# Performance work log

Measured on AMD Instinct MI355X. Metric: run time of the kernel, lower is better.

## Reference

```python
import jax, jax.numpy as jnp
import numpy as np

N_ATOMS = 100000
N_BONDS = 250000
MAX_NB = 6
HIDDEN = 256
DEPTH = 3
NUM_MOLS = 2000
ATOM_FDIM = 133
BOND_FDIM = 147


def setup_inputs() -> dict:
    key = jax.random.key(0)
    ks = jax.random.split(key, 12)
    return {
        "f_atoms": jax.random.normal(ks[0], (N_ATOMS, ATOM_FDIM), jnp.float32),
        "f_bonds": jax.random.normal(ks[1], (N_BONDS, BOND_FDIM), jnp.float32),
        "w_atoms": jax.random.uniform(ks[2], (N_ATOMS,), jnp.float32),
        "w_bonds": jax.random.uniform(ks[3], (N_BONDS,), jnp.float32),
        "W_i": jax.random.normal(ks[4], (BOND_FDIM, HIDDEN), jnp.float32) * 0.05,
        "W_h": jax.random.normal(ks[5], (HIDDEN, HIDDEN), jnp.float32) * 0.05,
        "W_o": jax.random.normal(ks[6], (ATOM_FDIM + HIDDEN, HIDDEN), jnp.float32) * 0.05,
        "b_o": jnp.zeros((HIDDEN,), jnp.float32),
        "degree_of_polym": jax.random.uniform(ks[7], (NUM_MOLS,), jnp.float32),
        "a2b": jax.random.randint(ks[8], (N_ATOMS, MAX_NB), 0, N_BONDS, jnp.int32),
        "b2a": jax.random.randint(ks[9], (N_BONDS,), 0, N_ATOMS, jnp.int32),
        "b2revb": jax.random.randint(ks[10], (N_BONDS,), 0, N_BONDS, jnp.int32),
        "mol_ids": jnp.sort(jax.random.randint(ks[11], (N_ATOMS,), 0, NUM_MOLS, jnp.int32)),
    }


def reference(f_atoms, f_bonds, w_atoms, w_bonds, W_i, W_h, W_o, b_o,
              degree_of_polym, a2b, b2a, b2revb, mol_ids):
    # input-layer: bond features -> hidden messages
    inp = f_bonds @ W_i                      # [n_bonds, H]
    message = jax.nn.relu(inp)

    for _ in range(DEPTH - 1):
        # gather incoming bond messages per atom and weight them
        nei_msg = message[a2b]               # [n_atoms, max_nb, H]
        nei_w = w_bonds[a2b]                 # [n_atoms, max_nb]
        a_message = (nei_msg * nei_w[..., None]).sum(axis=1)  # [n_atoms, H]
        # directed message: total at source atom minus reverse bond
        message = a_message[b2a] - message[b2revb]             # [n_bonds, H]
        message = jax.nn.relu(inp + message @ W_h)             # dropout p=0 (eval)

    # final atom-level readout
    nei_msg = message[a2b] * w_bonds[a2b][..., None]
    a_message = nei_msg.sum(axis=1)                            # [n_atoms, H]
    a_input = jnp.concatenate([f_atoms, a_message], axis=1)    # [n_atoms, atom_fdim+H]
    atom_hiddens = jax.nn.relu(a_input @ W_o + b_o)            # [n_atoms, H]

    # per-molecule weighted mean aggregation (a_scope loop -> segment_sum)
    weighted = atom_hiddens * w_atoms[:, None]
    mol_sum = jax.ops.segment_sum(weighted, mol_ids, num_segments=NUM_MOLS)
    w_sum = jax.ops.segment_sum(w_atoms, mol_ids, num_segments=NUM_MOLS)
    safe_w = jnp.where(w_sum > 0, w_sum, 1.0)
    mol_vecs = jnp.where((w_sum > 0)[:, None], mol_sum / safe_w[:, None], 0.0)
    mol_vecs = degree_of_polym[:, None] * mol_vecs             # [num_mols, H]
    return mol_vecs
```

## Files before the change

kernel.cpp:

```cpp
#include <hip/hip_runtime.h>
#include <hip/hip_bf16.h>

typedef unsigned short u16;
typedef __bf16 bf16x8v __attribute__((ext_vector_type(8)));
typedef float f32x4v __attribute__((ext_vector_type(4)));
typedef float f32x4u __attribute__((ext_vector_type(4))) __attribute__((aligned(4)));

__device__ __forceinline__ float bf2f(u16 u) {
    union { float f; unsigned int i; } c; c.i = ((unsigned int)u) << 16; return c.f;
}
__device__ __forceinline__ u16 f2bf(float f) {
    union { float f; unsigned int i; } c; c.f = f;
    unsigned int i = c.i;
    unsigned int lsb = (i >> 16) & 1u;
    i += 0x7fffu + lsb;
    return (u16)(i >> 16);
}
__device__ __forceinline__ float lo16(unsigned u) { return bf2f((u16)(u & 0xffff)); }
__device__ __forceinline__ float hi16(unsigned u) { return bf2f((u16)(u >> 16)); }
__device__ __forceinline__ unsigned pack2(float lo, float hi) {
    return (unsigned)f2bf(lo) | ((unsigned)f2bf(hi) << 16);
}

__device__ __forceinline__ unsigned neg2(unsigned u) { return u ^ 0x80008000u; }
__device__ __forceinline__ unsigned relu_neg2(unsigned u) {
    unsigned s = u & 0x80008000u;
    unsigned m = (s - (s >> 15)) | s;
    return (u ^ 0x80008000u) & ~m;
}

__device__ __forceinline__ bf16x8v load_cvt8(const float* __restrict__ rowp, int k, int kmax) {
    union { unsigned u[4]; bf16x8v v; } r;
#pragma unroll
    for (int g = 0; g < 2; ++g) {
        int kk = k + g * 4;
        float f0, f1, f2, f3;
        if (kk + 3 < kmax) {
            f32x4u q = *(const f32x4u*)(rowp + kk);
            f0 = q.x; f1 = q.y; f2 = q.z; f3 = q.w;
        } else {
            f0 = (kk + 0 < kmax) ? rowp[kk + 0] : 0.f;
            f1 = (kk + 1 < kmax) ? rowp[kk + 1] : 0.f;
            f2 = (kk + 2 < kmax) ? rowp[kk + 2] : 0.f;
            f3 = (kk + 3 < kmax) ? rowp[kk + 3] : 0.f;
        }
        r.u[g * 2]     = pack2(f0, f1);
        r.u[g * 2 + 1] = pack2(f2, f3);
    }
    return r.v;
}

__global__ __launch_bounds__(256)
void pack_all(const float* __restrict__ W_i, const float* __restrict__ W_h,
              const float* __restrict__ W_o,
              u16* __restrict__ wti, u16* __restrict__ wth, u16* __restrict__ wto) {
    int idx = blockIdx.x * 256 + threadIdx.x;
    if (idx < 256 * 160) {
        int n = idx / 160, k = idx % 160;
        wti[idx] = f2bf(k < 147 ? W_i[k * 256 + n] : 0.f);
        return;
    }
    idx -= 256 * 160;
    if (idx < 256 * 256) {
        int n = idx / 256, k = idx % 256;
        wth[idx] = f2bf(W_h[k * 256 + n]);
        return;
    }
    idx -= 256 * 256;
    if (idx < 256 * 448) {
        int n = idx / 448, k = idx % 448;
        float v;
        if (k < 256)       v = W_o[(133 + k) * 256 + n];
        else if (k < 389)  v = W_o[(k - 256) * 256 + n];
        else               v = 0.f;
        wto[idx] = f2bf(v);
    }
}

template <bool RELU>
__global__ __launch_bounds__(256)
void gather16(const u16* __restrict__ msg, const int* __restrict__ a2b,
              const float* __restrict__ w_bonds, u16* __restrict__ out, int nAtoms) {
    int t = threadIdx.x;
    int g = t >> 5;
    int co = (t & 31) * 8;
    int atom0 = blockIdx.x * 16 + g;
    int atom1 = atom0 + 8;
    if (atom1 >= nAtoms) { if (atom0 >= nAtoms) return; atom1 = atom0; }

    int bidx[12];
#pragma unroll
    for (int j = 0; j < 6; ++j) {
        bidx[j]     = a2b[atom0 * 6 + j];
        bidx[6 + j] = a2b[atom1 * 6 + j];
    }
    float w[12];
#pragma unroll
    for (int j = 0; j < 12; ++j) w[j] = w_bonds[bidx[j]];
    uint4 v[12];
#pragma unroll
    for (int j = 0; j < 12; ++j)
        v[j] = *(const uint4*)(msg + (size_t)bidx[j] * 256 + co);

    float a0[8] = {0,0,0,0,0,0,0,0}, a1[8] = {0,0,0,0,0,0,0,0};
#pragma unroll
    for (int j = 0; j < 6; ++j) {
        unsigned p[4] = {v[j].x, v[j].y, v[j].z, v[j].w};
        unsigned q[4] = {v[6+j].x, v[6+j].y, v[6+j].z, v[6+j].w};
#pragma unroll
        for (int c = 0; c < 4; ++c) {
            float m0 = lo16(p[c]), m1 = hi16(p[c]);
            float n0 = lo16(q[c]), n1 = hi16(q[c]);
            if (RELU) {
                m0 = fmaxf(m0, 0.f); m1 = fmaxf(m1, 0.f);
                n0 = fmaxf(n0, 0.f); n1 = fmaxf(n1, 0.f);
            }
            a0[c * 2]     += w[j] * m0;
            a0[c * 2 + 1] += w[j] * m1;
            a1[c * 2]     += w[6+j] * n0;
            a1[c * 2 + 1] += w[6+j] * n1;
        }
    }
    uint4 o0, o1;
    o0.x = pack2(a0[0], a0[1]); o0.y = pack2(a0[2], a0[3]);
    o0.z = pack2(a0[4], a0[5]); o0.w = pack2(a0[6], a0[7]);
    o1.x = pack2(a1[0], a1[1]); o1.y = pack2(a1[2], a1[3]);
    o1.z = pack2(a1[4], a1[5]); o1.w = pack2(a1[6], a1[7]);
    *(uint4*)(out + (size_t)atom0 * 256 + co) = o0;
    if (atom1 != atom0)
        *(uint4*)(out + (size_t)atom1 * 256 + co) = o1;
}

__global__ __launch_bounds__(512, 2)
void gemm_in(const float* __restrict__ A, const u16* __restrict__ Bt, int M,
             u16* __restrict__ out0) {
    constexpr int KPAD = 160, KMAX = 147, ASTR = 147;
    constexpr int LSTR = KPAD + 8;
    __shared__ u16 Bs[256 * LSTR];
    const int tid = threadIdx.x;
    const int wave = tid >> 6;
    const int lane = tid & 63;
    const int mrow = lane & 15;
    const int quad = lane >> 4;

    constexpr int KC = KPAD / 8;
    for (int i = tid; i < 256 * KC; i += 512) {
        int r = i / KC, kc = i % KC;
        *(uint4*)&Bs[r * LSTR + kc * 8] = *(const uint4*)&Bt[(size_t)r * KPAD + kc * 8];
    }
    __syncthreads();

    for (long chunk = blockIdx.x; chunk * 256 < (long)M; chunk += gridDim.x) {
        const long mbase = chunk * 256 + wave * 32;
        const float* rowp[2];
#pragma unroll
        for (int t = 0; t < 2; ++t) {
            long r = mbase + t * 16 + mrow;
            if (r >= M) r = M - 1;
            rowp[t] = A + r * ASTR;
        }

        f32x4v acc[2][16];
#pragma unroll
        for (int t = 0; t < 2; ++t)
#pragma unroll
            for (int j = 0; j < 16; ++j) acc[t][j] = (f32x4v){0.f, 0.f, 0.f, 0.f};

#pragma unroll 2
        for (int k0 = 0; k0 < KPAD; k0 += 32) {
            bf16x8v a_frag[2];
#pragma unroll
            for (int t = 0; t < 2; ++t)
                a_frag[t] = load_cvt8(rowp[t], k0 + quad * 8, KMAX);
#pragma unroll
            for (int jg = 0; jg < 4; ++jg) {
                bf16x8v b_frag[4];
#pragma unroll
                for (int j4 = 0; j4 < 4; ++j4)
                    b_frag[j4] = *(const bf16x8v*)&Bs[((jg * 4 + j4) * 16 + mrow) * LSTR + k0 + quad * 8];
#pragma unroll
                for (int t = 0; t < 2; ++t)
#pragma unroll
                    for (int j4 = 0; j4 < 4; ++j4)
                        acc[t][jg * 4 + j4] = __builtin_amdgcn_mfma_f32_16x16x32_bf16(
                            a_frag[t], b_frag[j4], acc[t][jg * 4 + j4], 0, 0, 0);
            }
        }

#pragma unroll
        for (int t = 0; t < 2; ++t)
#pragma unroll
            for (int r = 0; r < 4; ++r) {
                long grow = mbase + t * 16 + quad * 4 + r;
                if (grow < M)
#pragma unroll
                    for (int j = 0; j < 16; ++j)
                        out0[(size_t)grow * 256 + j * 16 + mrow] = f2bf(acc[t][j][r]);
            }
    }
}

template <bool RELUV>
__global__ __launch_bounds__(1024, 8)
void gemm_mp(const u16* __restrict__ amsg, const u16* __restrict__ msgsrc,
             const int* __restrict__ b2a, const int* __restrict__ b2revb,
             const u16* __restrict__ Bt, int M,
             const u16* __restrict__ inp, u16* __restrict__ out0) {
    constexpr int KPAD = 256;
    constexpr int LSTR = KPAD + 8;
    constexpr int NROWS = 128;
    __shared__ u16 Bs[NROWS * LSTR];
    const int tid = threadIdx.x;
    const int wave = tid >> 6;
    const int lane = tid & 63;
    const int mrow = lane & 15;
    const int quad = lane >> 4;

    const int nch = (M + 255) >> 8;
    const int cpx = (nch + 7) >> 3;
    const int bid = blockIdx.x;
    const int xcd = bid & 7;
    const int seq = bid >> 3;
    const long chunk = (long)xcd * cpx + (seq >> 1);
    if (chunk >= nch) return;
    const int nbase = (seq & 1) * NROWS;

    for (int i = tid; i < NROWS * 32; i += 1024) {
        int r = i >> 5, kc = i & 31;
        *(uint4*)&Bs[r * LSTR + kc * 8] = *(const uint4*)&Bt[(size_t)(nbase + r) * KPAD + kc * 8];
    }
    __syncthreads();

    const long mbase = chunk * 256 + wave * 16;
    long b = mbase + mrow;
    if (b >= M) b = M - 1;
    const size_t soff = (size_t)b2a[b] * 256 + quad * 8;
    const size_t roff = (size_t)b2revb[b] * 256 + quad * 8;

    f32x4v acc[8];
#pragma unroll
    for (int j = 0; j < 8; ++j) acc[j] = (f32x4v){0.f, 0.f, 0.f, 0.f};

#pragma unroll 2
    for (int k0 = 0; k0 < KPAD; k0 += 32) {
        uint4 va = *(const uint4*)&amsg[soff + k0];
        uint4 vr = *(const uint4*)&msgsrc[roff + k0];
        union { uint4 q; bf16x8v v; } ua, ur;
        ua.q = va;
        if (RELUV) {
            ur.q.x = relu_neg2(vr.x); ur.q.y = relu_neg2(vr.y);
            ur.q.z = relu_neg2(vr.z); ur.q.w = relu_neg2(vr.w);
        } else {
            ur.q.x = neg2(vr.x); ur.q.y = neg2(vr.y);
            ur.q.z = neg2(vr.z); ur.q.w = neg2(vr.w);
        }
#pragma unroll
        for (int j = 0; j < 8; ++j) {
            bf16x8v b_frag = *(const bf16x8v*)&Bs[(j * 16 + mrow) * LSTR + k0 + quad * 8];
            acc[j] = __builtin_amdgcn_mfma_f32_16x16x32_bf16(ua.v, b_frag, acc[j], 0, 0, 0);
            acc[j] = __builtin_amdgcn_mfma_f32_16x16x32_bf16(ur.v, b_frag, acc[j], 0, 0, 0);
        }
    }

#pragma unroll
    for (int r = 0; r < 4; ++r) {
        long grow = mbase + quad * 4 + r;
        if (grow < M)
#pragma unroll
            for (int j = 0; j < 8; ++j) {
                size_t idx = (size_t)grow * 256 + nbase + j * 16 + mrow;
                float s = bf2f(inp[idx]) + acc[j][r];
                out0[idx] = f2bf(s > 0.f ? s : 0.f);
            }
    }
}

__global__ __launch_bounds__(512, 2)
void gemm_ro(const u16* __restrict__ A1, const float* __restrict__ A2,
             const u16* __restrict__ Bt, int M,
             const float* __restrict__ bias, float* __restrict__ outf) {
    constexpr int KPAD = 448, KSPLIT = 256, K2 = 192, KMAX2 = 133;
    constexpr int LSTR = KPAD + 8;
    constexpr int NROWS = 128;
    __shared__ u16 Bs[NROWS * LSTR];
    const int tid = threadIdx.x;
    const int wave = tid >> 6;
    const int lane = tid & 63;
    const int mrow = lane & 15;
    const int quad = lane >> 4;

    const int nch = (M + 255) >> 8;
    const int cpx = (nch + 7) >> 3;
    const int bid = blockIdx.x;
    const int xcd = bid & 7;
    const int seq = bid >> 3;
    const long chunk = (long)xcd * cpx + (seq >> 1);
    if (chunk >= nch) return;
    const int nbase = (seq & 1) * NROWS;

    constexpr int KC = KPAD / 8;
    for (int i = tid; i < NROWS * KC; i += 512) {
        int r = i / KC, kc = i % KC;
        *(uint4*)&Bs[r * LSTR + kc * 8] =
            *(const uint4*)&Bt[(size_t)(nbase + r) * KPAD + kc * 8];
    }
    __syncthreads();

    const long mbase = chunk * 256 + wave * 32;
    long row[2];
#pragma unroll
    for (int t = 0; t < 2; ++t) {
        long r = mbase + t * 16 + mrow;
        if (r >= M) r = M - 1;
        row[t] = r;
    }

    f32x4v acc[2][8];
#pragma unroll
    for (int t = 0; t < 2; ++t)
#pragma unroll
        for (int j = 0; j < 8; ++j) acc[t][j] = (f32x4v){0.f, 0.f, 0.f, 0.f};

#pragma unroll 2
    for (int k0 = 0; k0 < KSPLIT; k0 += 32) {
        bf16x8v a_frag[2], b_frag[8];
#pragma unroll
        for (int t = 0; t < 2; ++t)
            a_frag[t] = *(const bf16x8v*)&A1[row[t] * KSPLIT + k0 + quad * 8];
#pragma unroll
        for (int j = 0; j < 8; ++j)
            b_frag[j] = *(const bf16x8v*)&Bs[(j * 16 + mrow) * LSTR + k0 + quad * 8];
#pragma unroll
        for (int t = 0; t < 2; ++t)
#pragma unroll
            for (int j = 0; j < 8; ++j)
                acc[t][j] = __builtin_amdgcn_mfma_f32_16x16x32_bf16(
                    a_frag[t], b_frag[j], acc[t][j], 0, 0, 0);
    }
#pragma unroll 2
    for (int k0 = 0; k0 < K2; k0 += 32) {
        bf16x8v a_frag[2], b_frag[8];
#pragma unroll
        for (int t = 0; t < 2; ++t)
            a_frag[t] = load_cvt8(A2 + row[t] * KMAX2, k0 + quad * 8, KMAX2);
#pragma unroll
        for (int j = 0; j < 8; ++j)
            b_frag[j] = *(const bf16x8v*)&Bs[(j * 16 + mrow) * LSTR + KSPLIT + k0 + quad * 8];
#pragma unroll
        for (int t = 0; t < 2; ++t)
#pragma unroll
            for (int j = 0; j < 8; ++j)
                acc[t][j] = __builtin_amdgcn_mfma_f32_16x16x32_bf16(
                    a_frag[t], b_frag[j], acc[t][j], 0, 0, 0);
    }

#pragma unroll
    for (int t = 0; t < 2; ++t)
#pragma unroll
        for (int r = 0; r < 4; ++r) {
            long grow = mbase + t * 16 + quad * 4 + r;
            if (grow < M)
#pragma unroll
                for (int j = 0; j < 8; ++j) {
                    int gcol = nbase + j * 16 + mrow;
                    float s = acc[t][j][r] + bias[gcol];
                    outf[(size_t)grow * 256 + gcol] = s > 0.f ? s : 0.f;
                }
        }
}

__global__ __launch_bounds__(256)
void aggregate_kernel(const float* __restrict__ hid, const float* __restrict__ w_atoms,
                      const int* __restrict__ mol_ids, const float* __restrict__ deg,
                      float* __restrict__ out, int nAtoms) {
    int m = blockIdx.x;
    int t = threadIdx.x;
    int lo = 0, hi = nAtoms;
    while (lo < hi) { int mid = (lo + hi) >> 1; if (mol_ids[mid] < m) lo = mid + 1; else hi = mid; }
    int start = lo;
    lo = start; hi = nAtoms;
    while (lo < hi) { int mid = (lo + hi) >> 1; if (mol_ids[mid] < m + 1) lo = mid + 1; else hi = mid; }
    int end = lo;
    float acc = 0.f, wsum = 0.f;
    for (int a = start; a < end; ++a) {
        float w = w_atoms[a];
        wsum += w;
        acc += w * hid[(size_t)a * 256 + t];
    }
    float res = (wsum > 0.f) ? deg[m] * acc / wsum : 0.f;
    out[m * 256 + t] = res;
}

extern "C" void kernel_launch(void* const* d_in, const int* in_sizes, int n_in,
                              void* d_out, int out_size, void* d_ws, size_t ws_size,
                              hipStream_t stream) {
    const float* f_atoms = (const float*)d_in[0];
    const float* f_bonds = (const float*)d_in[1];
    const float* w_atoms = (const float*)d_in[2];
    const float* w_bonds = (const float*)d_in[3];
    const float* W_i     = (const float*)d_in[4];
    const float* W_h     = (const float*)d_in[5];
    const float* W_o     = (const float*)d_in[6];
    const float* b_o     = (const float*)d_in[7];
    const float* deg     = (const float*)d_in[8];
    const int*   a2b     = (const int*)d_in[9];
    const int*   b2a     = (const int*)d_in[10];
    const int*   b2revb  = (const int*)d_in[11];
    const int*   mol_ids = (const int*)d_in[12];
    float* out = (float*)d_out;

    const int nB = 250000, nA = 100000, nM = 2000;

    char* ws = (char*)d_ws;
    u16* inp    = (u16*)(ws);
    u16* msgA   = (u16*)(ws + 128000000L);
    float* hid  = (float*)(ws + 256000000L);
    u16* amsg   = (u16*)(ws + 384000000L);
    u16* wt_i   = (u16*)(ws + 435200000L);
    u16* wt_h   = (u16*)(ws + 435200000L + 81920L);
    u16* wt_o   = (u16*)(ws + 435200000L + 81920L + 131072L);

    if (ws_size < 435642368UL) return;

    dim3 b256(256), b512(512), b1024(1024);
    pack_all<<<dim3((256 * 160 + 256 * 256 + 256 * 448 + 255) / 256), b256, 0, stream>>>(
        W_i, W_h, W_o, wt_i, wt_h, wt_o);

    gemm_in<<<dim3(977), b512, 0, stream>>>(f_bonds, wt_i, nB, inp);

    const int nchB = (nB + 255) >> 8, cpxB = (nchB + 7) >> 3;
    dim3 gmp(8 * cpxB * 2);
    const int nchA = (nA + 255) >> 8, cpxA = (nchA + 7) >> 3;
    dim3 gro(8 * cpxA * 2);

    gather16<true><<<dim3((nA + 15) / 16), b256, 0, stream>>>(inp, a2b, w_bonds, amsg, nA);
    gemm_mp<true><<<gmp, b1024, 0, stream>>>(
        amsg, inp, b2a, b2revb, wt_h, nB, inp, msgA);

    gather16<false><<<dim3((nA + 15) / 16), b256, 0, stream>>>(msgA, a2b, w_bonds, amsg, nA);
    gemm_mp<false><<<gmp, b1024, 0, stream>>>(
        amsg, msgA, b2a, b2revb, wt_h, nB, inp, inp);

    gather16<false><<<dim3((nA + 15) / 16), b256, 0, stream>>>(inp , a2b, w_bonds, amsg, nA);
    gemm_ro<<<gro, b512, 0, stream>>>(amsg, f_atoms, wt_o, nA, b_o, hid);

    aggregate_kernel<<<dim3(nM), b256, 0, stream>>>(hid, w_atoms, mol_ids, deg, out, nA);
}
```

Baseline: 851.1 us.

## Fuse per-molecule weighted sum into readout GEMM epilogue via atomics

The readout GEMM no longer writes the 100000x256 fp32 atom_hiddens buffer. Instead its epilogue weights each ReLU output by w_atoms and atomically adds it into a per-molecule sum, merging runs of rows in the same molecule before each atomic. The mol_sum buffer is zeroed inside the weight-packing kernel, and the final kernel only sums atom weights and divides. The W_o LDS tile is split into two phases so shared memory shrinks and launch bounds can rise to 4 blocks per CU. This trades a large global write and reread for atomic contention and an extra barrier and reload mid-kernel.

```diff
diff --git a/kernel.cpp b/kernel.cpp
--- a/kernel.cpp
+++ b/kernel.cpp
@@ -53,7 +53,8 @@
 __global__ __launch_bounds__(256)
 void pack_all(const float* __restrict__ W_i, const float* __restrict__ W_h,
               const float* __restrict__ W_o,
-              u16* __restrict__ wti, u16* __restrict__ wth, u16* __restrict__ wto) {
+              u16* __restrict__ wti, u16* __restrict__ wth, u16* __restrict__ wto,
+              float* __restrict__ mol_sum) {
     int idx = blockIdx.x * 256 + threadIdx.x;
     if (idx < 256 * 160) {
         int n = idx / 160, k = idx % 160;
@@ -74,7 +75,10 @@
         else if (k < 389)  v = W_o[(k - 256) * 256 + n];
         else               v = 0.f;
         wto[idx] = f2bf(v);
-    }
+        return;
+    }
+    idx -= 256 * 448;
+    if (idx < 2000 * 256) mol_sum[idx] = 0.f;
 }
 
 template <bool RELU>
@@ -275,12 +279,15 @@
     }
 }
 
-__global__ __launch_bounds__(512, 2)
+__global__ __launch_bounds__(512, 4)
 void gemm_ro(const u16* __restrict__ A1, const float* __restrict__ A2,
              const u16* __restrict__ Bt, int M,
-             const float* __restrict__ bias, float* __restrict__ outf) {
+             const float* __restrict__ bias,
+             const float* __restrict__ w_atoms, const int* __restrict__ mol_ids,
+             float* __restrict__ mol_sum) {
     constexpr int KPAD = 448, KSPLIT = 256, K2 = 192, KMAX2 = 133;
-    constexpr int LSTR = KPAD + 8;
+    constexpr int LSTR = KSPLIT + 8;
+    constexpr int LSTR2 = K2 + 8;
     constexpr int NROWS = 128;
     __shared__ u16 Bs[NROWS * LSTR];
     const int tid = threadIdx.x;
@@ -298,9 +305,8 @@
     if (chunk >= nch) return;
     const int nbase = (seq & 1) * NROWS;
 
-    constexpr int KC = KPAD / 8;
-    for (int i = tid; i < NROWS * KC; i += 512) {
-        int r = i / KC, kc = i % KC;
+    for (int i = tid; i < NROWS * 32; i += 512) {
+        int r = i >> 5, kc = i & 31;
         *(uint4*)&Bs[r * LSTR + kc * 8] =
             *(const uint4*)&Bt[(size_t)(nbase + r) * KPAD + kc * 8];
     }
@@ -323,56 +329,94 @@
 
 #pragma unroll 2
     for (int k0 = 0; k0 < KSPLIT; k0 += 32) {
-        bf16x8v a_frag[2], b_frag[8];
+        bf16x8v a_frag[2];
 #pragma unroll
         for (int t = 0; t < 2; ++t)
             a_frag[t] = *(const bf16x8v*)&A1[row[t] * KSPLIT + k0 + quad * 8];
 #pragma unroll
-        for (int j = 0; j < 8; ++j)
-            b_frag[j] = *(const bf16x8v*)&Bs[(j * 16 + mrow) * LSTR + k0 + quad * 8];
-#pragma unroll
-        for (int t = 0; t < 2; ++t)
-#pragma unroll
-            for (int j = 0; j < 8; ++j)
-                acc[t][j] = __builtin_amdgcn_mfma_f32_16x16x32_bf16(
-                    a_frag[t], b_frag[j], acc[t][j], 0, 0, 0);
-    }
+        for (int jg = 0; jg < 2; ++jg) {
+            bf16x8v b_frag[4];
+#pragma unroll
+            for (int j4 = 0; j4 < 4; ++j4)
+                b_frag[j4] = *(const bf16x8v*)&Bs[((jg * 4 + j4) * 16 + mrow) * LSTR + k0 + quad * 8];
+#pragma unroll
+            for (int t = 0; t < 2; ++t)
+#pragma unroll
+                for (int j4 = 0; j4 < 4; ++j4)
+                    acc[t][jg * 4 + j4] = __builtin_amdgcn_mfma_f32_16x16x32_bf16(
+                        a_frag[t], b_frag[j4], acc[t][jg * 4 + j4], 0, 0, 0);
+        }
+    }
+
+    __syncthreads();
+    for (int i = tid; i < NROWS * 24; i += 512) {
+        int r = i / 24, kc = i % 24;
+        *(uint4*)&Bs[r * LSTR2 + kc * 8] =
+            *(const uint4*)&Bt[(size_t)(nbase + r) * KPAD + KSPLIT + kc * 8];
+    }
+    __syncthreads();
+
 #pragma unroll 2
     for (int k0 = 0; k0 < K2; k0 += 32) {
-        bf16x8v a_frag[2], b_frag[8];
+        bf16x8v a_frag[2];
 #pragma unroll
         for (int t = 0; t < 2; ++t)
             a_frag[t] = load_cvt8(A2 + row[t] * KMAX2, k0 + quad * 8, KMAX2);
 #pragma unroll
-        for (int j = 0; j < 8; ++j)
-            b_frag[j] = *(const bf16x8v*)&Bs[(j * 16 + mrow) * LSTR + KSPLIT + k0 + quad * 8];
-#pragma unroll
-        for (int t = 0; t < 2; ++t)
-#pragma unroll
-            for (int j = 0; j < 8; ++j)
-                acc[t][j] = __builtin_amdgcn_mfma_f32_16x16x32_bf16(
-                    a_frag[t], b_frag[j], acc[t][j], 0, 0, 0);
-    }
-
-#pragma unroll
-    for (int t = 0; t < 2; ++t)
+        for (int jg = 0; jg < 2; ++jg) {
+            bf16x8v b_frag[4];
+#pragma unroll
+            for (int j4 = 0; j4 < 4; ++j4)
+                b_frag[j4] = *(const bf16x8v*)&Bs[((jg * 4 + j4) * 16 + mrow) * LSTR2 + k0 + quad * 8];
+#pragma unroll
+            for (int t = 0; t < 2; ++t)
+#pragma unroll
+                for (int j4 = 0; j4 < 4; ++j4)
+                    acc[t][jg * 4 + j4] = __builtin_amdgcn_mfma_f32_16x16x32_bf16(
+                        a_frag[t], b_frag[j4], acc[t][jg * 4 + j4], 0, 0, 0);
+        }
+    }
+
+#pragma unroll
+    for (int t = 0; t < 2; ++t) {
+        float w4[4]; int m4[4]; bool ok4[4];
 #pragma unroll
         for (int r = 0; r < 4; ++r) {
             long grow = mbase + t * 16 + quad * 4 + r;
-            if (grow < M)
-#pragma unroll
-                for (int j = 0; j < 8; ++j) {
-                    int gcol = nbase + j * 16 + mrow;
-                    float s = acc[t][j][r] + bias[gcol];
-                    outf[(size_t)grow * 256 + gcol] = s > 0.f ? s : 0.f;
+            ok4[r] = (grow < M);
+            long gr = ok4[r] ? grow : (M - 1);
+            w4[r] = w_atoms[gr];
+            m4[r] = mol_ids[gr];
+        }
+#pragma unroll
+        for (int j = 0; j < 8; ++j) {
+            int gcol = nbase + j * 16 + mrow;
+            float b = bias[gcol];
+            float vsum = 0.f;
+            int prev = -1;
+#pragma unroll
+            for (int r = 0; r < 4; ++r) {
+                if (ok4[r]) {
+                    float s = acc[t][j][r] + b;
+                    s = s > 0.f ? s : 0.f;
+                    float v = s * w4[r];
+                    if (m4[r] != prev) {
+                        if (prev >= 0) atomicAdd(&mol_sum[(size_t)prev * 256 + gcol], vsum);
+                        vsum = 0.f;
+                        prev = m4[r];
+                    }
+                    vsum += v;
                 }
-        }
+            }
+            if (prev >= 0) atomicAdd(&mol_sum[(size_t)prev * 256 + gcol], vsum);
+        }
+    }
 }
 
 __global__ __launch_bounds__(256)
-void aggregate_kernel(const float* __restrict__ hid, const float* __restrict__ w_atoms,
-                      const int* __restrict__ mol_ids, const float* __restrict__ deg,
-                      float* __restrict__ out, int nAtoms) {
+void finalize_kernel(const float* __restrict__ mol_sum, const float* __restrict__ w_atoms,
+                     const int* __restrict__ mol_ids, const float* __restrict__ deg,
+                     float* __restrict__ out, int nAtoms) {
     int m = blockIdx.x;
     int t = threadIdx.x;
     int lo = 0, hi = nAtoms;
@@ -381,13 +425,9 @@
     lo = start; hi = nAtoms;
     while (lo < hi) { int mid = (lo + hi) >> 1; if (mol_ids[mid] < m + 1) lo = mid + 1; else hi = mid; }
     int end = lo;
-    float acc = 0.f, wsum = 0.f;
-    for (int a = start; a < end; ++a) {
-        float w = w_atoms[a];
-        wsum += w;
-        acc += w * hid[(size_t)a * 256 + t];
-    }
-    float res = (wsum > 0.f) ? deg[m] * acc / wsum : 0.f;
+    float wsum = 0.f;
+    for (int a = start; a < end; ++a) wsum += w_atoms[a];
+    float res = (wsum > 0.f) ? deg[m] * mol_sum[(size_t)m * 256 + t] / wsum : 0.f;
     out[m * 256 + t] = res;
 }
 
@@ -412,19 +452,19 @@
     const int nB = 250000, nA = 100000, nM = 2000;
 
     char* ws = (char*)d_ws;
-    u16* inp    = (u16*)(ws);
-    u16* msgA   = (u16*)(ws + 128000000L);
-    float* hid  = (float*)(ws + 256000000L);
-    u16* amsg   = (u16*)(ws + 384000000L);
-    u16* wt_i   = (u16*)(ws + 435200000L);
-    u16* wt_h   = (u16*)(ws + 435200000L + 81920L);
-    u16* wt_o   = (u16*)(ws + 435200000L + 81920L + 131072L);
+    u16* inp      = (u16*)(ws);
+    u16* msgA     = (u16*)(ws + 128000000L);
+    float* mol_sum = (float*)(ws + 256000000L);
+    u16* amsg     = (u16*)(ws + 384000000L);
+    u16* wt_i     = (u16*)(ws + 435200000L);
+    u16* wt_h     = (u16*)(ws + 435200000L + 81920L);
+    u16* wt_o     = (u16*)(ws + 435200000L + 81920L + 131072L);
 
     if (ws_size < 435642368UL) return;
 
     dim3 b256(256), b512(512), b1024(1024);
-    pack_all<<<dim3((256 * 160 + 256 * 256 + 256 * 448 + 255) / 256), b256, 0, stream>>>(
-        W_i, W_h, W_o, wt_i, wt_h, wt_o);
+    pack_all<<<dim3(733184 / 256), b256, 0, stream>>>(
+        W_i, W_h, W_o, wt_i, wt_h, wt_o, mol_sum);
 
     gemm_in<<<dim3(977), b512, 0, stream>>>(f_bonds, wt_i, nB, inp);
 
@@ -442,7 +482,7 @@
         amsg, msgA, b2a, b2revb, wt_h, nB, inp, inp);
 
     gather16<false><<<dim3((nA + 15) / 16), b256, 0, stream>>>(inp , a2b, w_bonds, amsg, nA);
-    gemm_ro<<<gro, b512, 0, stream>>>(amsg, f_atoms, wt_o, nA, b_o, hid);
-
-    aggregate_kernel<<<dim3(nM), b256, 0, stream>>>(hid, w_atoms, mol_ids, deg, out, nA);
-}
+    gemm_ro<<<gro, b512, 0, stream>>>(amsg, f_atoms, wt_o, nA, b_o, w_atoms, mol_ids, mol_sum);
+
+    finalize_kernel<<<dim3(nM), b256, 0, stream>>>(mol_sum, w_atoms, mol_ids, deg, out, nA);
+}
```

After: 845.1 us. Within noise of the previous version (-0.7%).
